# Performance work log

Measured on AMD Instinct MI355X. Metric: run time of the kernel, lower is better.

The kernel has to match this reference:

```python
import jax, jax.numpy as jnp
import numpy as np

H = 64; W = 64          # input resolution
WS = 8                  # window size
SHIFT = 4               # shift size (= WS//2)
C = 384                 # dim
NH = 12                 # num heads
HD = C // NH            # head dim
HID = 4 * C             # mlp hidden
N = WS * WS             # tokens per window
NWIN = (H // WS) * (W // WS)
EPS = 1e-5


def _rel_pos_index():
    coords = np.stack(np.meshgrid(np.arange(WS), np.arange(WS), indexing='ij'))  # [2,WS,WS]
    flat = coords.reshape(2, -1)                                                 # [2,N]
    rel = flat[:, :, None] - flat[:, None, :]                                    # [2,N,N]
    rel = rel.transpose(1, 2, 0).copy()                                          # [N,N,2]
    rel[..., 0] += WS - 1
    rel[..., 1] += WS - 1
    rel[..., 0] *= 2 * WS - 1
    return rel.sum(-1)                                                           # [N,N]


def _attn_mask():
    img = np.zeros((H, W))
    cnt = 0
    for hs in (slice(0, -WS), slice(-WS, -SHIFT), slice(-SHIFT, None)):
        for ws_ in (slice(0, -WS), slice(-WS, -SHIFT), slice(-SHIFT, None)):
            img[hs, ws_] = cnt
            cnt += 1
    mw = img.reshape(H // WS, WS, W // WS, WS).transpose(0, 2, 1, 3).reshape(-1, N)  # [nW,N]
    diff = mw[:, None, :] - mw[:, :, None]                                           # [nW,N,N]
    return np.where(diff != 0, -100.0, 0.0).astype(np.float32)


_REL_IDX = jnp.asarray(_rel_pos_index())
_MASK = jnp.asarray(_attn_mask())


def _ln(x, g, b):
    m = jnp.mean(x, axis=-1, keepdims=True)
    v = jnp.mean((x - m) ** 2, axis=-1, keepdims=True)
    return (x - m) * jax.lax.rsqrt(v + EPS) * g + b


def _win_partition(x):
    # [B,H,W,C] -> [B*nW, N, C]
    B = x.shape[0]
    x = x.reshape(B, H // WS, WS, W // WS, WS, C).transpose(0, 1, 3, 2, 4, 5)
    return x.reshape(-1, N, C)


def _win_reverse(w, B):
    # [B*nW, N, C] -> [B,H,W,C]
    x = w.reshape(B, H // WS, W // WS, WS, WS, C).transpose(0, 1, 3, 2, 4, 5)
    return x.reshape(B, H, W, C)


def setup_inputs() -> dict:
    key = jax.random.key(0)
    ks = jax.random.split(key, 8)
    s = 0.02
    return {
        'x': jax.random.normal(ks[0], (32, H * W, C), jnp.float32),
        'gamma1': jnp.ones((C,), jnp.float32),
        'beta1': jnp.zeros((C,), jnp.float32),
        'w_qkv': jax.random.normal(ks[1], (C, 3 * C), jnp.float32) * s,
        'b_qkv': jnp.zeros((3 * C,), jnp.float32),
        'bias_table': jax.random.normal(ks[2], ((2 * WS - 1) ** 2, NH), jnp.float32) * s,
        'w_proj': jax.random.normal(ks[3], (C, C), jnp.float32) * s,
        'b_proj': jnp.zeros((C,), jnp.float32),
        'gamma2': jnp.ones((C,), jnp.float32),
        'beta2': jnp.zeros((C,), jnp.float32),
        'w_fc1': jax.random.normal(ks[4], (C, HID), jnp.float32) * s,
        'b_fc1': jnp.zeros((HID,), jnp.float32),
        'w_fc2': jax.random.normal(ks[5], (HID, C), jnp.float32) * s,
        'b_fc2': jnp.zeros((C,), jnp.float32),
    }


def reference(x, gamma1, beta1, w_qkv, b_qkv, bias_table, w_proj, b_proj,
              gamma2, beta2, w_fc1, b_fc1, w_fc2, b_fc2):
    B, L, _ = x.shape
    shortcut = x
    h = _ln(x, gamma1, beta1).reshape(B, H, W, C)
    h = jnp.roll(h, shift=(-SHIFT, -SHIFT), axis=(1, 2))
    xw = _win_partition(h)                                     # [B*nW, N, C]
    Bw = xw.shape[0]

    qkv = (xw @ w_qkv + b_qkv).reshape(Bw, N, 3, NH, HD)
    qkv = qkv.transpose(2, 0, 3, 1, 4)                         # [3, Bw, NH, N, HD]
    q, k, v = qkv[0], qkv[1], qkv[2]
    q = q * (HD ** -0.5)
    attn = jnp.einsum('bhnd,bhmd->bhnm', q, k)                 # [Bw, NH, N, N]

    rel_bias = bias_table[_REL_IDX.reshape(-1)].reshape(N, N, NH).transpose(2, 0, 1)
    attn = attn + rel_bias[None]
    attn = attn.reshape(B, NWIN, NH, N, N) + _MASK[None, :, None]
    attn = jax.nn.softmax(attn.reshape(Bw, NH, N, N), axis=-1)

    out = jnp.einsum('bhnm,bhmd->bhnd', attn, v)               # [Bw, NH, N, HD]
    out = out.transpose(0, 2, 1, 3).reshape(Bw, N, C)
    out = out @ w_proj + b_proj

    h = _win_reverse(out, B)
    h = jnp.roll(h, shift=(SHIFT, SHIFT), axis=(1, 2)).reshape(B, L, C)
    x = shortcut + h

    m = _ln(x, gamma2, beta2)
    m = jax.nn.gelu(m @ w_fc1 + b_fc1, approximate=False) @ w_fc2 + b_fc2
    return x + m
```

## Files before the change

kernel.cpp:

```cpp
#include <hip/hip_runtime.h>
#include <hip/hip_bf16.h>

typedef __bf16 bf16_t;
typedef __bf16 bf16x8 __attribute__((ext_vector_type(8)));
typedef float f32x4 __attribute__((ext_vector_type(4)));

#define DI __device__ __forceinline__

static constexpr int TOK = 131072;

DI int src_token(int t) {
  int b = t >> 12;
  int widx = (t >> 6) & 63;
  int n = t & 63;
  int wh = widx >> 3, ww = widx & 7;
  int i = n >> 3, j = n & 7;
  int y = ((wh << 3) + i + 4) & 63;
  int x2 = ((ww << 3) + j + 4) & 63;
  return (b << 12) + (y << 6) + x2;
}

DI f32x4 mfma16(bf16x8 a, bf16x8 b, f32x4 c) {
  return __builtin_amdgcn_mfma_f32_16x16x32_bf16(a, b, c, 0, 0, 0);
}

DI void gload_lds16(const bf16_t* g, bf16_t* l) {
  __builtin_amdgcn_global_load_lds(
      (__attribute__((address_space(1))) void*)const_cast<bf16_t*>(g),
      (__attribute__((address_space(3))) void*)l, 16, 0, 0);
}

__global__ void wconv_kernel(const float* __restrict__ w, bf16_t* __restrict__ wt,
                             int K, int N) {
  int idx = blockIdx.x * 256 + threadIdx.x;
  if (idx >= N * K) return;
  int n = idx / K, k = idx - n * K;
  wt[idx] = (bf16_t)w[(size_t)k * N + n];
}

template <int MAP>
__global__ __launch_bounds__(256)
void ln_kernel(const float* __restrict__ xin, const float* __restrict__ g,
               const float* __restrict__ be, bf16_t* __restrict__ out) {
  int w = threadIdx.x >> 6, l = threadIdx.x & 63;
  int t = blockIdx.x * 4 + w;
  int s = MAP ? src_token(t) : t;
  const float* row = xin + (size_t)s * 384;
  float v[6], s1 = 0.f, s2 = 0.f;
#pragma unroll
  for (int i = 0; i < 6; i++) {
    v[i] = row[l + i * 64];
    s1 += v[i];
    s2 += v[i] * v[i];
  }
#pragma unroll
  for (int o = 32; o; o >>= 1) {
    s1 += __shfl_xor(s1, o);
    s2 += __shfl_xor(s2, o);
  }
  float mean = s1 * (1.f / 384.f);
  float var = s2 * (1.f / 384.f) - mean * mean;
  float rs = rsqrtf(var + 1e-5f);
  bf16_t* orow = out + (size_t)t * 384;
#pragma unroll
  for (int i = 0; i < 6; i++) {
    int idx = l + i * 64;
    orow[idx] = (bf16_t)((v[i] - mean) * rs * g[idx] + be[idx]);
  }
}

template <int MODE>
__global__ __launch_bounds__(256, 2)
void gemm_bt(const bf16_t* __restrict__ A, const bf16_t* __restrict__ Wt,
             const float* __restrict__ bias, int K, int ldout,
             bf16_t* outb, float* outf, const float* resid) {
  __shared__ __align__(16) bf16_t Alds[128 * 32];
  __shared__ __align__(16) bf16_t Blds[128 * 32];
  const int tid = threadIdx.x;
  const int l = tid & 63, w = tid >> 6;
  const int lr = l & 15, lq = l >> 4;
  const int bn = blockIdx.x, bm = blockIdx.y;
  const int wr = w >> 1, wc = w & 1;
  const size_t rowA0 = (size_t)bm * 128, rowB0 = (size_t)bn * 128;

  f32x4 acc[4][4] = {};
  for (int k0 = 0; k0 < K; k0 += 32) {
#pragma unroll
    for (int r = 0; r < 2; r++) {
      int offb = r * 2048 + w * 512;
      int off = offb + l * 8;
      int row = off >> 5, col = off & 31;
      gload_lds16(A + (rowA0 + row) * K + k0 + col, &Alds[offb]);
      gload_lds16(Wt + (rowB0 + row) * K + k0 + col, &Blds[offb]);
    }
    __syncthreads();
    bf16x8 af[4], bfr[4];
#pragma unroll
    for (int fi = 0; fi < 4; fi++)
      af[fi] = *(const bf16x8*)&Alds[(wr * 64 + fi * 16 + lr) * 32 + lq * 8];
#pragma unroll
    for (int fj = 0; fj < 4; fj++)
      bfr[fj] = *(const bf16x8*)&Blds[(wc * 64 + fj * 16 + lr) * 32 + lq * 8];
#pragma unroll
    for (int fi = 0; fi < 4; fi++)
#pragma unroll
      for (int fj = 0; fj < 4; fj++)
        acc[fi][fj] = mfma16(af[fi], bfr[fj], acc[fi][fj]);
    __syncthreads();
  }

#pragma unroll
  for (int fi = 0; fi < 4; fi++) {
#pragma unroll
    for (int reg = 0; reg < 4; reg++) {
      int grow = bm * 128 + wr * 64 + fi * 16 + lq * 4 + reg;
      size_t rbase;
      if constexpr (MODE == 2)
        rbase = (size_t)src_token(grow) * ldout;
      else
        rbase = (size_t)grow * ldout;
#pragma unroll
      for (int fj = 0; fj < 4; fj++) {
        int gcol = bn * 128 + wc * 64 + fj * 16 + lr;
        float val = acc[fi][fj][reg] + bias[gcol];
        if constexpr (MODE == 0) {
          outb[rbase + gcol] = (bf16_t)val;
        } else if constexpr (MODE == 1) {
          val = 0.5f * val * (1.f + erff(val * 0.70710678118f));
          outb[rbase + gcol] = (bf16_t)val;
        } else {
          outf[rbase + gcol] = val + resid[rbase + gcol];
        }
      }
    }
  }
}

__global__ __launch_bounds__(64)
void attn_kernel(const bf16_t* __restrict__ qkv, const float* __restrict__ btab,
                 bf16_t* __restrict__ aout) {
  __shared__ __align__(16) bf16_t Qs[64 * 32];
  __shared__ __align__(16) bf16_t Ks[64 * 32];
  __shared__ __align__(16) bf16_t Vt[32 * 64];
  __shared__ __align__(16) bf16_t Ps[64 * 64];
  const int win = blockIdx.x, h = blockIdx.y;
  const int l = threadIdx.x;
  const int lr = l & 15, lq = l >> 4;

  {
    const bf16_t* qrow = qkv + ((size_t)win * 64 + l) * 1152 + h * 32;
#pragma unroll
    for (int c = 0; c < 4; c++) {
      *(bf16x8*)&Qs[l * 32 + c * 8] = *(const bf16x8*)&qrow[c * 8];
      *(bf16x8*)&Ks[l * 32 + c * 8] = *(const bf16x8*)&qrow[384 + c * 8];
    }
#pragma unroll
    for (int c = 0; c < 4; c++) {
      bf16x8 tv = *(const bf16x8*)&qrow[768 + c * 8];
#pragma unroll
      for (int e = 0; e < 8; e++) Vt[(c * 8 + e) * 64 + l] = tv[e];
    }
  }
  __syncthreads();

  f32x4 sacc[4][4] = {};
  {
    bf16x8 a[4], b[4];
#pragma unroll
    for (int fi = 0; fi < 4; fi++)
      a[fi] = *(const bf16x8*)&Qs[(fi * 16 + lr) * 32 + lq * 8];
#pragma unroll
    for (int fj = 0; fj < 4; fj++)
      b[fj] = *(const bf16x8*)&Ks[(fj * 16 + lr) * 32 + lq * 8];
#pragma unroll
    for (int fi = 0; fi < 4; fi++)
#pragma unroll
      for (int fj = 0; fj < 4; fj++)
        sacc[fi][fj] = mfma16(a[fi], b[fj], sacc[fi][fj]);
  }

  const int widx = win & 63;
  const int wh = widx >> 3, ww = widx & 7;
  const float scale = 0.17677669529663687f;
#pragma unroll
  for (int fi = 0; fi < 4; fi++) {
#pragma unroll
    for (int reg = 0; reg < 4; reg++) {
      int row = fi * 16 + lq * 4 + reg;
      int i1 = row >> 3, j1 = row & 7;
      int ly1 = (wh == 7) ? (i1 >= 4 ? 2 : 1) : 0;
      int lx1 = (ww == 7) ? (j1 >= 4 ? 2 : 1) : 0;
      float vals[4], m = -1e30f;
#pragma unroll
      for (int fj = 0; fj < 4; fj++) {
        int col = fj * 16 + lr;
        int i2 = col >> 3, j2 = col & 7;
        float v = sacc[fi][fj][reg] * scale +
                  btab[((i1 - i2 + 7) * 15 + (j1 - j2 + 7)) * 12 + h];
        int ly2 = (wh == 7) ? (i2 >= 4 ? 2 : 1) : 0;
        int lx2 = (ww == 7) ? (j2 >= 4 ? 2 : 1) : 0;
        if (ly1 != ly2 || lx1 != lx2) v -= 100.f;
        vals[fj] = v;
        m = fmaxf(m, v);
      }
#pragma unroll
      for (int o = 1; o < 16; o <<= 1) m = fmaxf(m, __shfl_xor(m, o));
      float ssum = 0.f;
#pragma unroll
      for (int fj = 0; fj < 4; fj++) {
        vals[fj] = __expf(vals[fj] - m);
        ssum += vals[fj];
      }
#pragma unroll
      for (int o = 1; o < 16; o <<= 1) ssum += __shfl_xor(ssum, o);
      float inv = 1.f / ssum;
#pragma unroll
      for (int fj = 0; fj < 4; fj++)
        Ps[row * 64 + fj * 16 + lr] = (bf16_t)(vals[fj] * inv);
    }
  }
  __syncthreads();

  f32x4 oacc[4][2] = {};
#pragma unroll
  for (int kc = 0; kc < 2; kc++) {
    bf16x8 pa[4], vb[2];
#pragma unroll
    for (int fi = 0; fi < 4; fi++)
      pa[fi] = *(const bf16x8*)&Ps[(fi * 16 + lr) * 64 + kc * 32 + lq * 8];
#pragma unroll
    for (int fj = 0; fj < 2; fj++)
      vb[fj] = *(const bf16x8*)&Vt[(fj * 16 + lr) * 64 + kc * 32 + lq * 8];
#pragma unroll
    for (int fi = 0; fi < 4; fi++)
#pragma unroll
      for (int fj = 0; fj < 2; fj++)
        oacc[fi][fj] = mfma16(pa[fi], vb[fj], oacc[fi][fj]);
  }
#pragma unroll
  for (int fi = 0; fi < 4; fi++)
#pragma unroll
    for (int reg = 0; reg < 4; reg++) {
      int row = fi * 16 + lq * 4 + reg;
      size_t rb = ((size_t)win * 64 + row) * 384 + h * 32;
#pragma unroll
      for (int fj = 0; fj < 2; fj++)
        aout[rb + fj * 16 + lr] = (bf16_t)oacc[fi][fj][reg];
    }
}

extern "C" void kernel_launch(void* const* d_in, const int* in_sizes, int n_in,
                              void* d_out, int out_size, void* d_ws, size_t ws_size,
                              hipStream_t stream) {
  (void)in_sizes; (void)n_in; (void)out_size; (void)ws_size;
  const float* x      = (const float*)d_in[0];
  const float* gamma1 = (const float*)d_in[1];
  const float* beta1  = (const float*)d_in[2];
  const float* w_qkv  = (const float*)d_in[3];
  const float* b_qkv  = (const float*)d_in[4];
  const float* btab   = (const float*)d_in[5];
  const float* w_proj = (const float*)d_in[6];
  const float* b_proj = (const float*)d_in[7];
  const float* gamma2 = (const float*)d_in[8];
  const float* beta2  = (const float*)d_in[9];
  const float* w_fc1  = (const float*)d_in[10];
  const float* b_fc1  = (const float*)d_in[11];
  const float* w_fc2  = (const float*)d_in[12];
  const float* b_fc2  = (const float*)d_in[13];
  float* out = (float*)d_out;

  char* ws = (char*)d_ws;
  size_t off = 0;
  auto alloc = [&](size_t bytes) {
    void* p = ws + off;
    off += (bytes + 255) & ~(size_t)255;
    return p;
  };
  bf16_t* wqkvT  = (bf16_t*)alloc((size_t)1152 * 384 * 2);
  bf16_t* wprojT = (bf16_t*)alloc((size_t)384 * 384 * 2);
  bf16_t* wfc1T  = (bf16_t*)alloc((size_t)1536 * 384 * 2);
  bf16_t* wfc2T  = (bf16_t*)alloc((size_t)384 * 1536 * 2);
  bf16_t* bufA   = (bf16_t*)alloc((size_t)TOK * 1536 * 2);
  bf16_t* bufB   = (bf16_t*)alloc((size_t)TOK * 384 * 2);

  wconv_kernel<<<(1152 * 384 + 255) / 256, 256, 0, stream>>>(w_qkv, wqkvT, 384, 1152);
  wconv_kernel<<<(384 * 384 + 255) / 256, 256, 0, stream>>>(w_proj, wprojT, 384, 384);
  wconv_kernel<<<(384 * 1536 + 255) / 256, 256, 0, stream>>>(w_fc1, wfc1T, 384, 1536);
  wconv_kernel<<<(1536 * 384 + 255) / 256, 256, 0, stream>>>(w_fc2, wfc2T, 1536, 384);

  ln_kernel<1><<<TOK / 4, 256, 0, stream>>>(x, gamma1, beta1, bufB);
  gemm_bt<0><<<dim3(1152 / 128, TOK / 128), 256, 0, stream>>>(
      bufB, wqkvT, b_qkv, 384, 1152, bufA, nullptr, nullptr);
  attn_kernel<<<dim3(2048, 12), 64, 0, stream>>>(bufA, btab, bufB);
  gemm_bt<2><<<dim3(384 / 128, TOK / 128), 256, 0, stream>>>(
      bufB, wprojT, b_proj, 384, 384, nullptr, out, x);
  ln_kernel<0><<<TOK / 4, 256, 0, stream>>>(out, gamma2, beta2, bufB);
  gemm_bt<1><<<dim3(1536 / 128, TOK / 128), 256, 0, stream>>>(
      bufB, wfc1T, b_fc1, 384, 1536, bufA, nullptr, nullptr);
  gemm_bt<3><<<dim3(384 / 128, TOK / 128), 256, 0, stream>>>(
      bufA, wfc2T, b_fc2, 1536, 384, nullptr, out, out);
}
```

Baseline: 1.345 ms.

## Emit head-major Q/K/Vᵀ from QKV GEMM and double-buffer GEMM LDS tiles

The QKV GEMM epilogue now scatters its output directly into per-head, per-window Q, K and transposed V buffers, with Q pre-scaled. The attention kernel can then load its MFMA fragments straight from global memory instead of staging and transposing through LDS. The shared GEMM kernel also double-buffers its LDS tiles so the next K-slice loads while the current one computes, and drops the minimum-occupancy launch bound. The probability matrix in LDS gets an XOR swizzle to reduce bank conflicts. The trade-off is that the transposed V stores are narrow, strided writes, and the doubled LDS may lower occupancy.

```diff
diff --git a/kernel.cpp b/kernel.cpp
--- a/kernel.cpp
+++ b/kernel.cpp
@@ -8,6 +8,7 @@
 #define DI __device__ __forceinline__
 
 static constexpr int TOK = 131072;
+static constexpr int NWIN = 2048;
 
 DI int src_token(int t) {
   int b = t >> 12;
@@ -70,12 +71,13 @@
 }
 
 template <int MODE>
-__global__ __launch_bounds__(256, 2)
+__global__ __launch_bounds__(256)
 void gemm_bt(const bf16_t* __restrict__ A, const bf16_t* __restrict__ Wt,
              const float* __restrict__ bias, int K, int ldout,
-             bf16_t* outb, float* outf, const float* resid) {
-  __shared__ __align__(16) bf16_t Alds[128 * 32];
-  __shared__ __align__(16) bf16_t Blds[128 * 32];
+             bf16_t* outb, float* outf, const float* resid,
+             bf16_t* qout, bf16_t* kout, bf16_t* vout) {
+  __shared__ __align__(16) bf16_t Alds[2][128 * 32];
+  __shared__ __align__(16) bf16_t Blds[2][128 * 32];
   const int tid = threadIdx.x;
   const int l = tid & 63, w = tid >> 6;
   const int lr = l & 15, lq = l >> 4;
@@ -83,24 +85,32 @@
   const int wr = w >> 1, wc = w & 1;
   const size_t rowA0 = (size_t)bm * 128, rowB0 = (size_t)bn * 128;
 
-  f32x4 acc[4][4] = {};
-  for (int k0 = 0; k0 < K; k0 += 32) {
+  auto stage = [&](int buf, int ki) {
+    int k0 = ki << 5;
 #pragma unroll
     for (int r = 0; r < 2; r++) {
       int offb = r * 2048 + w * 512;
       int off = offb + l * 8;
       int row = off >> 5, col = off & 31;
-      gload_lds16(A + (rowA0 + row) * K + k0 + col, &Alds[offb]);
-      gload_lds16(Wt + (rowB0 + row) * K + k0 + col, &Blds[offb]);
-    }
-    __syncthreads();
+      gload_lds16(A + (rowA0 + row) * K + k0 + col, &Alds[buf][offb]);
+      gload_lds16(Wt + (rowB0 + row) * K + k0 + col, &Blds[buf][offb]);
+    }
+  };
+
+  const int nk = K >> 5;
+  f32x4 acc[4][4] = {};
+  stage(0, 0);
+  __syncthreads();
+  for (int ki = 0; ki < nk; ki++) {
+    int cur = ki & 1;
+    if (ki + 1 < nk) stage(cur ^ 1, ki + 1);
     bf16x8 af[4], bfr[4];
 #pragma unroll
     for (int fi = 0; fi < 4; fi++)
-      af[fi] = *(const bf16x8*)&Alds[(wr * 64 + fi * 16 + lr) * 32 + lq * 8];
+      af[fi] = *(const bf16x8*)&Alds[cur][(wr * 64 + fi * 16 + lr) * 32 + lq * 8];
 #pragma unroll
     for (int fj = 0; fj < 4; fj++)
-      bfr[fj] = *(const bf16x8*)&Blds[(wc * 64 + fj * 16 + lr) * 32 + lq * 8];
+      bfr[fj] = *(const bf16x8*)&Blds[cur][(wc * 64 + fj * 16 + lr) * 32 + lq * 8];
 #pragma unroll
     for (int fi = 0; fi < 4; fi++)
 #pragma unroll
@@ -123,13 +133,23 @@
       for (int fj = 0; fj < 4; fj++) {
         int gcol = bn * 128 + wc * 64 + fj * 16 + lr;
         float val = acc[fi][fj][reg] + bias[gcol];
-        if constexpr (MODE == 0) {
-          outb[rbase + gcol] = (bf16_t)val;
-        } else if constexpr (MODE == 1) {
+        if constexpr (MODE == 1) {
           val = 0.5f * val * (1.f + erff(val * 0.70710678118f));
           outb[rbase + gcol] = (bf16_t)val;
+        } else if constexpr (MODE == 2 || MODE == 3) {
+          outf[rbase + gcol] = val + resid[rbase + gcol];
         } else {
-          outf[rbase + gcol] = val + resid[rbase + gcol];
+          int sel = gcol / 384;
+          int rem = gcol - sel * 384;
+          int h = rem >> 5, d = rem & 31;
+          int win = grow >> 6, tok = grow & 63;
+          size_t wb = (size_t)h * NWIN + win;
+          if (sel == 0)
+            qout[(wb * 64 + tok) * 32 + d] = (bf16_t)(val * 0.17677669529663687f);
+          else if (sel == 1)
+            kout[(wb * 64 + tok) * 32 + d] = (bf16_t)val;
+          else
+            vout[(wb * 32 + d) * 64 + tok] = (bf16_t)val;
         }
       }
     }
@@ -137,41 +157,24 @@
 }
 
 __global__ __launch_bounds__(64)
-void attn_kernel(const bf16_t* __restrict__ qkv, const float* __restrict__ btab,
+void attn_kernel(const bf16_t* __restrict__ Qb, const bf16_t* __restrict__ Kb,
+                 const bf16_t* __restrict__ Vb, const float* __restrict__ btab,
                  bf16_t* __restrict__ aout) {
-  __shared__ __align__(16) bf16_t Qs[64 * 32];
-  __shared__ __align__(16) bf16_t Ks[64 * 32];
-  __shared__ __align__(16) bf16_t Vt[32 * 64];
   __shared__ __align__(16) bf16_t Ps[64 * 64];
-  const int win = blockIdx.x, h = blockIdx.y;
-  const int l = threadIdx.x;
-  const int lr = l & 15, lq = l >> 4;
-
-  {
-    const bf16_t* qrow = qkv + ((size_t)win * 64 + l) * 1152 + h * 32;
-#pragma unroll
-    for (int c = 0; c < 4; c++) {
-      *(bf16x8*)&Qs[l * 32 + c * 8] = *(const bf16x8*)&qrow[c * 8];
-      *(bf16x8*)&Ks[l * 32 + c * 8] = *(const bf16x8*)&qrow[384 + c * 8];
-    }
-#pragma unroll
-    for (int c = 0; c < 4; c++) {
-      bf16x8 tv = *(const bf16x8*)&qrow[768 + c * 8];
-#pragma unroll
-      for (int e = 0; e < 8; e++) Vt[(c * 8 + e) * 64 + l] = tv[e];
-    }
-  }
-  __syncthreads();
+  const int bid = blockIdx.x;
+  const int win = bid & (NWIN - 1), h = bid >> 11;
+  const int l = threadIdx.x, lr = l & 15, lq = l >> 4;
+  const size_t base = ((size_t)h * NWIN + win) * 2048;
 
   f32x4 sacc[4][4] = {};
   {
     bf16x8 a[4], b[4];
 #pragma unroll
     for (int fi = 0; fi < 4; fi++)
-      a[fi] = *(const bf16x8*)&Qs[(fi * 16 + lr) * 32 + lq * 8];
+      a[fi] = *(const bf16x8*)&Qb[base + (fi * 16 + lr) * 32 + lq * 8];
 #pragma unroll
     for (int fj = 0; fj < 4; fj++)
-      b[fj] = *(const bf16x8*)&Ks[(fj * 16 + lr) * 32 + lq * 8];
+      b[fj] = *(const bf16x8*)&Kb[base + (fj * 16 + lr) * 32 + lq * 8];
 #pragma unroll
     for (int fi = 0; fi < 4; fi++)
 #pragma unroll
@@ -181,7 +184,6 @@
 
   const int widx = win & 63;
   const int wh = widx >> 3, ww = widx & 7;
-  const float scale = 0.17677669529663687f;
 #pragma unroll
   for (int fi = 0; fi < 4; fi++) {
 #pragma unroll
@@ -195,7 +197,7 @@
       for (int fj = 0; fj < 4; fj++) {
         int col = fj * 16 + lr;
         int i2 = col >> 3, j2 = col & 7;
-        float v = sacc[fi][fj][reg] * scale +
+        float v = sacc[fi][fj][reg] +
                   btab[((i1 - i2 + 7) * 15 + (j1 - j2 + 7)) * 12 + h];
         int ly2 = (wh == 7) ? (i2 >= 4 ? 2 : 1) : 0;
         int lx2 = (ww == 7) ? (j2 >= 4 ? 2 : 1) : 0;
@@ -214,9 +216,10 @@
 #pragma unroll
       for (int o = 1; o < 16; o <<= 1) ssum += __shfl_xor(ssum, o);
       float inv = 1.f / ssum;
+      int sw = (row & 7) << 3;
 #pragma unroll
       for (int fj = 0; fj < 4; fj++)
-        Ps[row * 64 + fj * 16 + lr] = (bf16_t)(vals[fj] * inv);
+        Ps[row * 64 + ((fj * 16 + lr) ^ sw)] = (bf16_t)(vals[fj] * inv);
     }
   }
   __syncthreads();
@@ -226,11 +229,13 @@
   for (int kc = 0; kc < 2; kc++) {
     bf16x8 pa[4], vb[2];
 #pragma unroll
-    for (int fi = 0; fi < 4; fi++)
-      pa[fi] = *(const bf16x8*)&Ps[(fi * 16 + lr) * 64 + kc * 32 + lq * 8];
+    for (int fi = 0; fi < 4; fi++) {
+      int row = fi * 16 + lr;
+      pa[fi] = *(const bf16x8*)&Ps[row * 64 + ((kc * 32 + lq * 8) ^ ((row & 7) << 3))];
+    }
 #pragma unroll
     for (int fj = 0; fj < 2; fj++)
-      vb[fj] = *(const bf16x8*)&Vt[(fj * 16 + lr) * 64 + kc * 32 + lq * 8];
+      vb[fj] = *(const bf16x8*)&Vb[base + (fj * 16 + lr) * 64 + kc * 32 + lq * 8];
 #pragma unroll
     for (int fi = 0; fi < 4; fi++)
 #pragma unroll
@@ -280,8 +285,12 @@
   bf16_t* wprojT = (bf16_t*)alloc((size_t)384 * 384 * 2);
   bf16_t* wfc1T  = (bf16_t*)alloc((size_t)1536 * 384 * 2);
   bf16_t* wfc2T  = (bf16_t*)alloc((size_t)384 * 1536 * 2);
-  bf16_t* bufA   = (bf16_t*)alloc((size_t)TOK * 1536 * 2);
-  bf16_t* bufB   = (bf16_t*)alloc((size_t)TOK * 384 * 2);
+  char* big = (char*)alloc((size_t)TOK * 1536 * 2);
+  bf16_t* qb = (bf16_t*)big;
+  bf16_t* kb = (bf16_t*)(big + (size_t)12 * NWIN * 2048 * 2);
+  bf16_t* vb = (bf16_t*)(big + (size_t)24 * NWIN * 2048 * 2);
+  bf16_t* bufH = (bf16_t*)big;
+  bf16_t* bufB = (bf16_t*)alloc((size_t)TOK * 384 * 2);
 
   wconv_kernel<<<(1152 * 384 + 255) / 256, 256, 0, stream>>>(w_qkv, wqkvT, 384, 1152);
   wconv_kernel<<<(384 * 384 + 255) / 256, 256, 0, stream>>>(w_proj, wprojT, 384, 384);
@@ -289,14 +298,14 @@
   wconv_kernel<<<(1536 * 384 + 255) / 256, 256, 0, stream>>>(w_fc2, wfc2T, 1536, 384);
 
   ln_kernel<1><<<TOK / 4, 256, 0, stream>>>(x, gamma1, beta1, bufB);
-  gemm_bt<0><<<dim3(1152 / 128, TOK / 128), 256, 0, stream>>>(
-      bufB, wqkvT, b_qkv, 384, 1152, bufA, nullptr, nullptr);
-  attn_kernel<<<dim3(2048, 12), 64, 0, stream>>>(bufA, btab, bufB);
+  gemm_bt<4><<<dim3(1152 / 128, TOK / 128), 256, 0, stream>>>(
+      bufB, wqkvT, b_qkv, 384, 0, nullptr, nullptr, nullptr, qb, kb, vb);
+  attn_kernel<<<NWIN * 12, 64, 0, stream>>>(qb, kb, vb, btab, bufB);
   gemm_bt<2><<<dim3(384 / 128, TOK / 128), 256, 0, stream>>>(
-      bufB, wprojT, b_proj, 384, 384, nullptr, out, x);
+      bufB, wprojT, b_proj, 384, 384, nullptr, out, x, nullptr, nullptr, nullptr);
   ln_kernel<0><<<TOK / 4, 256, 0, stream>>>(out, gamma2, beta2, bufB);
   gemm_bt<1><<<dim3(1536 / 128, TOK / 128), 256, 0, stream>>>(
-      bufB, wfc1T, b_fc1, 384, 1536, bufA, nullptr, nullptr);
+      bufB, wfc1T, b_fc1, 384, 1536, bufH, nullptr, nullptr, nullptr, nullptr, nullptr);
   gemm_bt<3><<<dim3(384 / 128, TOK / 128), 256, 0, stream>>>(
-      bufA, wfc2T, b_fc2, 1536, 384, nullptr, out, out);
-}
+      bufH, wfc2T, b_fc2, 1536, 384, nullptr, out, out, nullptr, nullptr, nullptr);
+}
```

Result: slower. 1.527 ms (+13.5%).

## Widen GEMM tiles to 384-column strips, fuse LN2 into proj epilogue, swizzle attention LDS

Applied to the files above, without the earlier changes.

The 128x128 GEMM becomes a 512-thread kernel that computes 128x384 strips, so each A tile is loaded once for up to 384 output columns. The proj GEMM now computes the full 384-wide row itself, so its epilogue adds the residual and computes LayerNorm2 through a shared-memory reduction. That removes the separate LN pass and its re-read of the fp32 activations. The MLP stays in window order and scatters back through src_token at fc2. The attention kernel XOR-swizzles the P and V-transpose LDS layouts to cut bank conflicts. The trade-off is higher register and LDS use per block, which may lower occupancy.

```diff
diff --git a/kernel.cpp b/kernel.cpp
--- a/kernel.cpp
+++ b/kernel.cpp
@@ -8,6 +8,7 @@
 #define DI __device__ __forceinline__
 
 static constexpr int TOK = 131072;
+static constexpr int NWIN = 2048;
 
 DI int src_token(int t) {
   int b = t >> 12;
@@ -38,13 +39,12 @@
   wt[idx] = (bf16_t)w[(size_t)k * N + n];
 }
 
-template <int MAP>
 __global__ __launch_bounds__(256)
 void ln_kernel(const float* __restrict__ xin, const float* __restrict__ g,
                const float* __restrict__ be, bf16_t* __restrict__ out) {
   int w = threadIdx.x >> 6, l = threadIdx.x & 63;
   int t = blockIdx.x * 4 + w;
-  int s = MAP ? src_token(t) : t;
+  int s = src_token(t);
   const float* row = xin + (size_t)s * 384;
   float v[6], s1 = 0.f, s2 = 0.f;
 #pragma unroll
@@ -70,41 +70,46 @@
 }
 
 template <int MODE>
-__global__ __launch_bounds__(256, 2)
-void gemm_bt(const bf16_t* __restrict__ A, const bf16_t* __restrict__ Wt,
-             const float* __restrict__ bias, int K, int ldout,
-             bf16_t* outb, float* outf, const float* resid) {
+__global__ __launch_bounds__(512, 2)
+void gemm_strip(const bf16_t* __restrict__ A, const bf16_t* __restrict__ Wt,
+                const float* __restrict__ bias, int K, int ldout,
+                bf16_t* outb, float* outf, const float* resid,
+                const float* g2, const float* b2, bf16_t* lnout) {
   __shared__ __align__(16) bf16_t Alds[128 * 32];
-  __shared__ __align__(16) bf16_t Blds[128 * 32];
+  __shared__ __align__(16) bf16_t Blds[384 * 32];
+  __shared__ float lnred[128][8];
   const int tid = threadIdx.x;
   const int l = tid & 63, w = tid >> 6;
   const int lr = l & 15, lq = l >> 4;
   const int bn = blockIdx.x, bm = blockIdx.y;
-  const int wr = w >> 1, wc = w & 1;
-  const size_t rowA0 = (size_t)bm * 128, rowB0 = (size_t)bn * 128;
-
-  f32x4 acc[4][4] = {};
+  const int wr = w >> 2, wc = w & 3;
+  const size_t rowA0 = (size_t)bm * 128, rowB0 = (size_t)bn * 384;
+
+  f32x4 acc[4][6] = {};
   for (int k0 = 0; k0 < K; k0 += 32) {
-#pragma unroll
-    for (int r = 0; r < 2; r++) {
-      int offb = r * 2048 + w * 512;
+    {
+      int offb = w * 512;
       int off = offb + l * 8;
-      int row = off >> 5, col = off & 31;
-      gload_lds16(A + (rowA0 + row) * K + k0 + col, &Alds[offb]);
-      gload_lds16(Wt + (rowB0 + row) * K + k0 + col, &Blds[offb]);
+      gload_lds16(A + (rowA0 + (off >> 5)) * K + k0 + (off & 31), &Alds[offb]);
+    }
+#pragma unroll
+    for (int p = 0; p < 3; p++) {
+      int offb = p * 4096 + w * 512;
+      int off = offb + l * 8;
+      gload_lds16(Wt + (rowB0 + (off >> 5)) * K + k0 + (off & 31), &Blds[offb]);
     }
     __syncthreads();
-    bf16x8 af[4], bfr[4];
+    bf16x8 af[4], bfr[6];
 #pragma unroll
     for (int fi = 0; fi < 4; fi++)
       af[fi] = *(const bf16x8*)&Alds[(wr * 64 + fi * 16 + lr) * 32 + lq * 8];
 #pragma unroll
-    for (int fj = 0; fj < 4; fj++)
-      bfr[fj] = *(const bf16x8*)&Blds[(wc * 64 + fj * 16 + lr) * 32 + lq * 8];
-#pragma unroll
-    for (int fi = 0; fi < 4; fi++)
-#pragma unroll
-      for (int fj = 0; fj < 4; fj++)
+    for (int fj = 0; fj < 6; fj++)
+      bfr[fj] = *(const bf16x8*)&Blds[(wc * 96 + fj * 16 + lr) * 32 + lq * 8];
+#pragma unroll
+    for (int fi = 0; fi < 4; fi++)
+#pragma unroll
+      for (int fj = 0; fj < 6; fj++)
         acc[fi][fj] = mfma16(af[fi], bfr[fj], acc[fi][fj]);
     __syncthreads();
   }
@@ -113,23 +118,65 @@
   for (int fi = 0; fi < 4; fi++) {
 #pragma unroll
     for (int reg = 0; reg < 4; reg++) {
-      int grow = bm * 128 + wr * 64 + fi * 16 + lq * 4 + reg;
-      size_t rbase;
-      if constexpr (MODE == 2)
-        rbase = (size_t)src_token(grow) * ldout;
-      else
-        rbase = (size_t)grow * ldout;
-#pragma unroll
-      for (int fj = 0; fj < 4; fj++) {
-        int gcol = bn * 128 + wc * 64 + fj * 16 + lr;
-        float val = acc[fi][fj][reg] + bias[gcol];
-        if constexpr (MODE == 0) {
+      int lrow = wr * 64 + fi * 16 + lq * 4 + reg;
+      int grow = bm * 128 + lrow;
+      if constexpr (MODE == 0 || MODE == 1) {
+        size_t rbase = (size_t)grow * ldout;
+#pragma unroll
+        for (int fj = 0; fj < 6; fj++) {
+          int gcol = bn * 384 + wc * 96 + fj * 16 + lr;
+          float val = acc[fi][fj][reg] + bias[gcol];
+          if constexpr (MODE == 1)
+            val = 0.5f * val * (1.f + erff(val * 0.70710678118f));
           outb[rbase + gcol] = (bf16_t)val;
-        } else if constexpr (MODE == 1) {
-          val = 0.5f * val * (1.f + erff(val * 0.70710678118f));
-          outb[rbase + gcol] = (bf16_t)val;
-        } else {
-          outf[rbase + gcol] = val + resid[rbase + gcol];
+        }
+      } else if constexpr (MODE == 2) {
+        size_t obase = (size_t)src_token(grow) * 384;
+        float s1 = 0.f, s2 = 0.f;
+#pragma unroll
+        for (int fj = 0; fj < 6; fj++) {
+          int c = wc * 96 + fj * 16 + lr;
+          float x1 = acc[fi][fj][reg] + bias[c] + resid[obase + c];
+          outf[obase + c] = x1;
+          acc[fi][fj][reg] = x1;
+          s1 += x1;
+          s2 += x1 * x1;
+        }
+#pragma unroll
+        for (int o = 1; o < 16; o <<= 1) {
+          s1 += __shfl_xor(s1, o);
+          s2 += __shfl_xor(s2, o);
+        }
+        if (lr == 0) {
+          lnred[lrow][wc * 2] = s1;
+          lnred[lrow][wc * 2 + 1] = s2;
+        }
+      } else {
+        size_t obase = (size_t)src_token(grow) * 384;
+#pragma unroll
+        for (int fj = 0; fj < 6; fj++) {
+          int c = wc * 96 + fj * 16 + lr;
+          outf[obase + c] = acc[fi][fj][reg] + bias[c] + resid[obase + c];
+        }
+      }
+    }
+  }
+  if constexpr (MODE == 2) {
+    __syncthreads();
+#pragma unroll
+    for (int fi = 0; fi < 4; fi++) {
+#pragma unroll
+      for (int reg = 0; reg < 4; reg++) {
+        int lrow = wr * 64 + fi * 16 + lq * 4 + reg;
+        int grow = bm * 128 + lrow;
+        float m = (lnred[lrow][0] + lnred[lrow][2] + lnred[lrow][4] + lnred[lrow][6]) * (1.f / 384.f);
+        float v = (lnred[lrow][1] + lnred[lrow][3] + lnred[lrow][5] + lnred[lrow][7]) * (1.f / 384.f) - m * m;
+        float rs = rsqrtf(v + 1e-5f);
+#pragma unroll
+        for (int fj = 0; fj < 6; fj++) {
+          int c = wc * 96 + fj * 16 + lr;
+          lnout[(size_t)grow * 384 + c] =
+              (bf16_t)((acc[fi][fj][reg] - m) * rs * g2[c] + b2[c]);
         }
       }
     }
@@ -144,8 +191,7 @@
   __shared__ __align__(16) bf16_t Vt[32 * 64];
   __shared__ __align__(16) bf16_t Ps[64 * 64];
   const int win = blockIdx.x, h = blockIdx.y;
-  const int l = threadIdx.x;
-  const int lr = l & 15, lq = l >> 4;
+  const int l = threadIdx.x, lr = l & 15, lq = l >> 4;
 
   {
     const bf16_t* qrow = qkv + ((size_t)win * 64 + l) * 1152 + h * 32;
@@ -158,7 +204,10 @@
     for (int c = 0; c < 4; c++) {
       bf16x8 tv = *(const bf16x8*)&qrow[768 + c * 8];
 #pragma unroll
-      for (int e = 0; e < 8; e++) Vt[(c * 8 + e) * 64 + l] = tv[e];
+      for (int e = 0; e < 8; e++) {
+        int vr = c * 8 + e;
+        Vt[vr * 64 + (l ^ ((vr & 7) << 3))] = tv[e];
+      }
     }
   }
   __syncthreads();
@@ -214,9 +263,10 @@
 #pragma unroll
       for (int o = 1; o < 16; o <<= 1) ssum += __shfl_xor(ssum, o);
       float inv = 1.f / ssum;
+      int sw = (row & 7) << 3;
 #pragma unroll
       for (int fj = 0; fj < 4; fj++)
-        Ps[row * 64 + fj * 16 + lr] = (bf16_t)(vals[fj] * inv);
+        Ps[row * 64 + ((fj * 16 + lr) ^ sw)] = (bf16_t)(vals[fj] * inv);
     }
   }
   __syncthreads();
@@ -226,11 +276,15 @@
   for (int kc = 0; kc < 2; kc++) {
     bf16x8 pa[4], vb[2];
 #pragma unroll
-    for (int fi = 0; fi < 4; fi++)
-      pa[fi] = *(const bf16x8*)&Ps[(fi * 16 + lr) * 64 + kc * 32 + lq * 8];
-#pragma unroll
-    for (int fj = 0; fj < 2; fj++)
-      vb[fj] = *(const bf16x8*)&Vt[(fj * 16 + lr) * 64 + kc * 32 + lq * 8];
+    for (int fi = 0; fi < 4; fi++) {
+      int row = fi * 16 + lr;
+      pa[fi] = *(const bf16x8*)&Ps[row * 64 + ((kc * 32 + lq * 8) ^ ((row & 7) << 3))];
+    }
+#pragma unroll
+    for (int fj = 0; fj < 2; fj++) {
+      int row = fj * 16 + lr;
+      vb[fj] = *(const bf16x8*)&Vt[row * 64 + ((kc * 32 + lq * 8) ^ ((row & 7) << 3))];
+    }
 #pragma unroll
     for (int fi = 0; fi < 4; fi++)
 #pragma unroll
@@ -280,23 +334,24 @@
   bf16_t* wprojT = (bf16_t*)alloc((size_t)384 * 384 * 2);
   bf16_t* wfc1T  = (bf16_t*)alloc((size_t)1536 * 384 * 2);
   bf16_t* wfc2T  = (bf16_t*)alloc((size_t)384 * 1536 * 2);
-  bf16_t* bufA   = (bf16_t*)alloc((size_t)TOK * 1536 * 2);
-  bf16_t* bufB   = (bf16_t*)alloc((size_t)TOK * 384 * 2);
+  char* big = (char*)alloc((size_t)TOK * 1536 * 2);
+  bf16_t* bufA = (bf16_t*)big;
+  bf16_t* bufH = (bf16_t*)big;
+  bf16_t* bufB = (bf16_t*)alloc((size_t)TOK * 384 * 2);
 
   wconv_kernel<<<(1152 * 384 + 255) / 256, 256, 0, stream>>>(w_qkv, wqkvT, 384, 1152);
   wconv_kernel<<<(384 * 384 + 255) / 256, 256, 0, stream>>>(w_proj, wprojT, 384, 384);
   wconv_kernel<<<(384 * 1536 + 255) / 256, 256, 0, stream>>>(w_fc1, wfc1T, 384, 1536);
   wconv_kernel<<<(1536 * 384 + 255) / 256, 256, 0, stream>>>(w_fc2, wfc2T, 1536, 384);
 
-  ln_kernel<1><<<TOK / 4, 256, 0, stream>>>(x, gamma1, beta1, bufB);
-  gemm_bt<0><<<dim3(1152 / 128, TOK / 128), 256, 0, stream>>>(
-      bufB, wqkvT, b_qkv, 384, 1152, bufA, nullptr, nullptr);
-  attn_kernel<<<dim3(2048, 12), 64, 0, stream>>>(bufA, btab, bufB);
-  gemm_bt<2><<<dim3(384 / 128, TOK / 128), 256, 0, stream>>>(
-      bufB, wprojT, b_proj, 384, 384, nullptr, out, x);
-  ln_kernel<0><<<TOK / 4, 256, 0, stream>>>(out, gamma2, beta2, bufB);
-  gemm_bt<1><<<dim3(1536 / 128, TOK / 128), 256, 0, stream>>>(
-      bufB, wfc1T, b_fc1, 384, 1536, bufA, nullptr, nullptr);
-  gemm_bt<3><<<dim3(384 / 128, TOK / 128), 256, 0, stream>>>(
-      bufA, wfc2T, b_fc2, 1536, 384, nullptr, out, out);
-}
+  ln_kernel<<<TOK / 4, 256, 0, stream>>>(x, gamma1, beta1, bufB);
+  gemm_strip<0><<<dim3(3, TOK / 128), 512, 0, stream>>>(
+      bufB, wqkvT, b_qkv, 384, 1152, bufA, nullptr, nullptr, nullptr, nullptr, nullptr);
+  attn_kernel<<<dim3(NWIN, 12), 64, 0, stream>>>(bufA, btab, bufB);
+  gemm_strip<2><<<dim3(1, TOK / 128), 512, 0, stream>>>(
+      bufB, wprojT, b_proj, 384, 384, nullptr, out, x, gamma2, beta2, bufB);
+  gemm_strip<1><<<dim3(4, TOK / 128), 512, 0, stream>>>(
+      bufB, wfc1T, b_fc1, 384, 1536, bufH, nullptr, nullptr, nullptr, nullptr, nullptr);
+  gemm_strip<3><<<dim3(1, TOK / 128), 512, 0, stream>>>(
+      bufH, wfc2T, b_fc2, 1536, 384, nullptr, out, out, nullptr, nullptr, nullptr);
+}
```

Result: slower. 1.713 ms (+27.3%).

## Swizzle LDS layouts, widen GEMM K-tile to 64, raise occupancy hint

Applied to the files above, without the earlier changes.

The GEMM K-step is doubled to 64 so each barrier pair covers two MFMA sub-steps. An XOR swizzle on the LDS row layout is applied both to the direct-to-LDS global loads and to the fragment reads, to cut bank conflicts. The attention kernel's V-transpose and probability tiles get the same swizzle, and the launch bound asks for 4 blocks per SM. LDS per block doubles to 32KB, which the higher occupancy target must fit alongside register pressure.

```diff
diff --git a/kernel.cpp b/kernel.cpp
--- a/kernel.cpp
+++ b/kernel.cpp
@@ -8,6 +8,7 @@
 #define DI __device__ __forceinline__
 
 static constexpr int TOK = 131072;
+static constexpr int NWIN = 2048;
 
 DI int src_token(int t) {
   int b = t >> 12;
@@ -70,12 +71,12 @@
 }
 
 template <int MODE>
-__global__ __launch_bounds__(256, 2)
+__global__ __launch_bounds__(256, 4)
 void gemm_bt(const bf16_t* __restrict__ A, const bf16_t* __restrict__ Wt,
              const float* __restrict__ bias, int K, int ldout,
              bf16_t* outb, float* outf, const float* resid) {
-  __shared__ __align__(16) bf16_t Alds[128 * 32];
-  __shared__ __align__(16) bf16_t Blds[128 * 32];
+  __shared__ __align__(16) bf16_t Alds[128 * 64];
+  __shared__ __align__(16) bf16_t Blds[128 * 64];
   const int tid = threadIdx.x;
   const int l = tid & 63, w = tid >> 6;
   const int lr = l & 15, lq = l >> 4;
@@ -84,28 +85,39 @@
   const size_t rowA0 = (size_t)bm * 128, rowB0 = (size_t)bn * 128;
 
   f32x4 acc[4][4] = {};
-  for (int k0 = 0; k0 < K; k0 += 32) {
-#pragma unroll
-    for (int r = 0; r < 2; r++) {
+  for (int k0 = 0; k0 < K; k0 += 64) {
+#pragma unroll
+    for (int r = 0; r < 4; r++) {
       int offb = r * 2048 + w * 512;
       int off = offb + l * 8;
-      int row = off >> 5, col = off & 31;
-      gload_lds16(A + (rowA0 + row) * K + k0 + col, &Alds[offb]);
-      gload_lds16(Wt + (rowB0 + row) * K + k0 + col, &Blds[offb]);
+      int row = off >> 6;
+      int slot = (off >> 3) & 7;
+      int scol = (slot ^ (row & 7)) << 3;
+      gload_lds16(A + (rowA0 + row) * K + k0 + scol, &Alds[offb]);
+      gload_lds16(Wt + (rowB0 + row) * K + k0 + scol, &Blds[offb]);
     }
     __syncthreads();
-    bf16x8 af[4], bfr[4];
-#pragma unroll
-    for (int fi = 0; fi < 4; fi++)
-      af[fi] = *(const bf16x8*)&Alds[(wr * 64 + fi * 16 + lr) * 32 + lq * 8];
-#pragma unroll
-    for (int fj = 0; fj < 4; fj++)
-      bfr[fj] = *(const bf16x8*)&Blds[(wc * 64 + fj * 16 + lr) * 32 + lq * 8];
-#pragma unroll
-    for (int fi = 0; fi < 4; fi++)
-#pragma unroll
-      for (int fj = 0; fj < 4; fj++)
-        acc[fi][fj] = mfma16(af[fi], bfr[fj], acc[fi][fj]);
+#pragma unroll
+    for (int ks = 0; ks < 2; ks++) {
+      bf16x8 af[4], bfr[4];
+#pragma unroll
+      for (int fi = 0; fi < 4; fi++) {
+        int row = wr * 64 + fi * 16 + lr;
+        af[fi] = *(const bf16x8*)&Alds[row * 64 +
+                                       ((ks * 32 + lq * 8) ^ ((row & 7) << 3))];
+      }
+#pragma unroll
+      for (int fj = 0; fj < 4; fj++) {
+        int row = wc * 64 + fj * 16 + lr;
+        bfr[fj] = *(const bf16x8*)&Blds[row * 64 +
+                                        ((ks * 32 + lq * 8) ^ ((row & 7) << 3))];
+      }
+#pragma unroll
+      for (int fi = 0; fi < 4; fi++)
+#pragma unroll
+        for (int fj = 0; fj < 4; fj++)
+          acc[fi][fj] = mfma16(af[fi], bfr[fj], acc[fi][fj]);
+    }
     __syncthreads();
   }
 
@@ -144,8 +156,7 @@
   __shared__ __align__(16) bf16_t Vt[32 * 64];
   __shared__ __align__(16) bf16_t Ps[64 * 64];
   const int win = blockIdx.x, h = blockIdx.y;
-  const int l = threadIdx.x;
-  const int lr = l & 15, lq = l >> 4;
+  const int l = threadIdx.x, lr = l & 15, lq = l >> 4;
 
   {
     const bf16_t* qrow = qkv + ((size_t)win * 64 + l) * 1152 + h * 32;
@@ -158,7 +169,10 @@
     for (int c = 0; c < 4; c++) {
       bf16x8 tv = *(const bf16x8*)&qrow[768 + c * 8];
 #pragma unroll
-      for (int e = 0; e < 8; e++) Vt[(c * 8 + e) * 64 + l] = tv[e];
+      for (int e = 0; e < 8; e++) {
+        int vr = c * 8 + e;
+        Vt[vr * 64 + (l ^ ((vr & 7) << 3))] = tv[e];
+      }
     }
   }
   __syncthreads();
@@ -214,9 +228,10 @@
 #pragma unroll
       for (int o = 1; o < 16; o <<= 1) ssum += __shfl_xor(ssum, o);
       float inv = 1.f / ssum;
+      int sw = (row & 7) << 3;
 #pragma unroll
       for (int fj = 0; fj < 4; fj++)
-        Ps[row * 64 + fj * 16 + lr] = (bf16_t)(vals[fj] * inv);
+        Ps[row * 64 + ((fj * 16 + lr) ^ sw)] = (bf16_t)(vals[fj] * inv);
     }
   }
   __syncthreads();
@@ -226,11 +241,15 @@
   for (int kc = 0; kc < 2; kc++) {
     bf16x8 pa[4], vb[2];
 #pragma unroll
-    for (int fi = 0; fi < 4; fi++)
-      pa[fi] = *(const bf16x8*)&Ps[(fi * 16 + lr) * 64 + kc * 32 + lq * 8];
-#pragma unroll
-    for (int fj = 0; fj < 2; fj++)
-      vb[fj] = *(const bf16x8*)&Vt[(fj * 16 + lr) * 64 + kc * 32 + lq * 8];
+    for (int fi = 0; fi < 4; fi++) {
+      int row = fi * 16 + lr;
+      pa[fi] = *(const bf16x8*)&Ps[row * 64 + ((kc * 32 + lq * 8) ^ ((row & 7) << 3))];
+    }
+#pragma unroll
+    for (int fj = 0; fj < 2; fj++) {
+      int row = fj * 16 + lr;
+      vb[fj] = *(const bf16x8*)&Vt[row * 64 + ((kc * 32 + lq * 8) ^ ((row & 7) << 3))];
+    }
 #pragma unroll
     for (int fi = 0; fi < 4; fi++)
 #pragma unroll
@@ -280,8 +299,10 @@
   bf16_t* wprojT = (bf16_t*)alloc((size_t)384 * 384 * 2);
   bf16_t* wfc1T  = (bf16_t*)alloc((size_t)1536 * 384 * 2);
   bf16_t* wfc2T  = (bf16_t*)alloc((size_t)384 * 1536 * 2);
-  bf16_t* bufA   = (bf16_t*)alloc((size_t)TOK * 1536 * 2);
-  bf16_t* bufB   = (bf16_t*)alloc((size_t)TOK * 384 * 2);
+  char* big = (char*)alloc((size_t)TOK * 1536 * 2);
+  bf16_t* bufA = (bf16_t*)big;
+  bf16_t* bufH = (bf16_t*)big;
+  bf16_t* bufB = (bf16_t*)alloc((size_t)TOK * 384 * 2);
 
   wconv_kernel<<<(1152 * 384 + 255) / 256, 256, 0, stream>>>(w_qkv, wqkvT, 384, 1152);
   wconv_kernel<<<(384 * 384 + 255) / 256, 256, 0, stream>>>(w_proj, wprojT, 384, 384);
@@ -291,12 +312,12 @@
   ln_kernel<1><<<TOK / 4, 256, 0, stream>>>(x, gamma1, beta1, bufB);
   gemm_bt<0><<<dim3(1152 / 128, TOK / 128), 256, 0, stream>>>(
       bufB, wqkvT, b_qkv, 384, 1152, bufA, nullptr, nullptr);
-  attn_kernel<<<dim3(2048, 12), 64, 0, stream>>>(bufA, btab, bufB);
+  attn_kernel<<<dim3(NWIN, 12), 64, 0, stream>>>(bufA, btab, bufB);
   gemm_bt<2><<<dim3(384 / 128, TOK / 128), 256, 0, stream>>>(
       bufB, wprojT, b_proj, 384, 384, nullptr, out, x);
   ln_kernel<0><<<TOK / 4, 256, 0, stream>>>(out, gamma2, beta2, bufB);
   gemm_bt<1><<<dim3(1536 / 128, TOK / 128), 256, 0, stream>>>(
-      bufB, wfc1T, b_fc1, 384, 1536, bufA, nullptr, nullptr);
+      bufB, wfc1T, b_fc1, 384, 1536, bufH, nullptr, nullptr);
   gemm_bt<3><<<dim3(384 / 128, TOK / 128), 256, 0, stream>>>(
-      bufA, wfc2T, b_fc2, 1536, 384, nullptr, out, out);
-}
+      bufH, wfc2T, b_fc2, 1536, 384, nullptr, out, out);
+}
```

After: 1.249 ms. 7.2% less time.
